# Performance work log

Hardware: AMD Instinct MI355X
Metric: run time of the kernel (lower is better)

Reference implementation:

```python
import jax, jax.numpy as jnp
import numpy as np

HIDDEN = 2048
N_HEADS = 16
N_KV_HEADS = 4
HEAD_DIM = HIDDEN // N_HEADS  # 128
BATCH = 2
SEQ = 2048


def setup_inputs() -> dict:
    key = jax.random.key(0)
    ks = jax.random.split(key, 10)
    s = 0.02
    return {
        "hidden_states": jax.random.normal(ks[0], (BATCH, SEQ, HIDDEN), jnp.float32),
        "attention_mask": jnp.ones((BATCH, SEQ), jnp.int32),
        # weights stored [in, out] so y = x @ W + b (transpose of torch layout)
        "Wq": jax.random.normal(ks[1], (HIDDEN, N_HEADS * HEAD_DIM), jnp.float32) * s,
        "bq": jnp.zeros((N_HEADS * HEAD_DIM,), jnp.float32),
        "Wk": jax.random.normal(ks[2], (HIDDEN, N_KV_HEADS * HEAD_DIM), jnp.float32) * s,
        "bk": jnp.zeros((N_KV_HEADS * HEAD_DIM,), jnp.float32),
        "Wv": jax.random.normal(ks[3], (HIDDEN, N_KV_HEADS * HEAD_DIM), jnp.float32) * s,
        "bv": jnp.zeros((N_KV_HEADS * HEAD_DIM,), jnp.float32),
        "Wo": jax.random.normal(ks[4], (N_HEADS * HEAD_DIM, HIDDEN), jnp.float32) * s,
        "bo": jnp.zeros((HIDDEN,), jnp.float32),
    }


def reference(hidden_states, attention_mask, Wq, bq, Wk, bk, Wv, bv, Wo, bo):
    B, S, _ = hidden_states.shape
    q = hidden_states @ Wq + bq  # [B,S,H*D]
    k = hidden_states @ Wk + bk  # [B,S,Hkv*D]
    v = hidden_states @ Wv + bv

    q = q.reshape(B, S, N_HEADS, HEAD_DIM).transpose(0, 2, 1, 3)      # [B,H,S,D]
    k = k.reshape(B, S, N_KV_HEADS, HEAD_DIM).transpose(0, 2, 1, 3)   # [B,Hkv,S,D]
    v = v.reshape(B, S, N_KV_HEADS, HEAD_DIM).transpose(0, 2, 1, 3)

    # GQA: repeat_interleave along head dim (head h uses kv head h // groups)
    groups = N_HEADS // N_KV_HEADS
    k = jnp.repeat(k, groups, axis=1)  # [B,H,S,D]
    v = jnp.repeat(v, groups, axis=1)

    scale = 1.0 / np.sqrt(HEAD_DIM)
    scores = jnp.einsum('bhqd,bhkd->bhqk', q, k) * scale  # [B,H,S,S]

    causal = jnp.tril(jnp.ones((S, S), bool))              # True = keep
    keep = causal[None, None, :, :] & (attention_mask[:, None, None, :] != 0)
    scores = jnp.where(keep, scores, -jnp.inf)

    attn = jax.nn.softmax(scores.astype(jnp.float32), axis=-1).astype(q.dtype)
    out = jnp.einsum('bhqk,bhkd->bhqd', attn, v)            # [B,H,S,D]
    out = out.transpose(0, 2, 1, 3).reshape(B, S, N_HEADS * HEAD_DIM)
    return out @ Wo + bo
```

## Files before the change

kernel.cpp:

```cpp
#include <hip/hip_runtime.h>
#include <hip/hip_bf16.h>


typedef unsigned short u16;
typedef unsigned long long u64;
typedef __attribute__((ext_vector_type(8))) short short8;
typedef __attribute__((ext_vector_type(4))) float f32x4;
typedef __attribute__((ext_vector_type(4))) unsigned uint4v;

#define BATCH 2
#define SEQ 2048
#define HIDDEN 2048
#define NH 16
#define NKV 4
#define HD 128
#define QKV_N 3072
#define MROWS 4096

__device__ inline u16 f2bf(float f) {
    __hip_bfloat16 h = __float2bfloat16(f);
    return __builtin_bit_cast(u16, h);
}

__device__ inline void async_copy16(const u16* g, u16* lds_base) {
    __builtin_amdgcn_global_load_lds(
        (const __attribute__((address_space(1))) void*)g,
        (__attribute__((address_space(3))) void*)lds_base, 16, 0, 0);
}

#define PREP_CONV   8192
#define PREP_WQ     (PREP_CONV + 4096)
#define PREP_WK     (PREP_WQ + 1024)
#define PREP_WV     (PREP_WK + 1024)
#define PREP_WO     (PREP_WV + 4096)
#define PREP_BIAS   (PREP_WO + 12)
#define PREP_TOTAL  (PREP_BIAS + 1)

__device__ inline void prep_transpose(const float* __restrict__ src, u16* __restrict__ dst,
                                      int N, int sub, float (*tile)[33]) {
    int nx = N >> 5;
    int bx = sub % nx, by = sub / nx;
    int n0 = bx * 32, k0 = by * 32;
    int t = threadIdx.x, tx = t & 31, ty = t >> 5;
#pragma unroll
    for (int i = 0; i < 32; i += 8)
        tile[ty + i][tx] = src[(size_t)(k0 + ty + i) * N + n0 + tx];
    __syncthreads();
#pragma unroll
    for (int i = 0; i < 32; i += 8)
        dst[(size_t)(n0 + ty + i) * HIDDEN + k0 + tx] = f2bf(tile[tx][ty + i]);
}

__global__ __launch_bounds__(256)
void prep(const float* __restrict__ hidden, u16* __restrict__ xb,
          const float* __restrict__ Wq, const float* __restrict__ Wk,
          const float* __restrict__ Wv, const float* __restrict__ Wo,
          u16* __restrict__ wqkvT, u16* __restrict__ woT,
          const float* __restrict__ bq, const float* __restrict__ bk,
          const float* __restrict__ bv, float* __restrict__ bqkv,
          const int* __restrict__ am, u64* __restrict__ mp) {
    __shared__ float tile[32][33];
    int bid = blockIdx.x;
    if (bid < PREP_CONV) {
        int i = (bid * 256 + threadIdx.x) * 4;
        float4 v = *(const float4*)(hidden + i);
        ushort4 o;
        o.x = f2bf(v.x); o.y = f2bf(v.y); o.z = f2bf(v.z); o.w = f2bf(v.w);
        *(ushort4*)(xb + i) = o;
    } else if (bid < PREP_WQ) {
        prep_transpose(Wq, wqkvT, 2048, bid - PREP_CONV, tile);
    } else if (bid < PREP_WK) {
        prep_transpose(Wk, wqkvT + (size_t)2048 * HIDDEN, 512, bid - PREP_WQ, tile);
    } else if (bid < PREP_WV) {
        prep_transpose(Wv, wqkvT + (size_t)2560 * HIDDEN, 512, bid - PREP_WK, tile);
    } else if (bid < PREP_WO) {
        prep_transpose(Wo, woT, 2048, bid - PREP_WV, tile);
    } else if (bid < PREP_BIAS) {
        int i = (bid - PREP_WO) * 256 + threadIdx.x;
        if (i < QKV_N)
            bqkv[i] = (i < 2048) ? bq[i] : ((i < 2560) ? bk[i - 2048] : bv[i - 2560]);
    } else {
        int i = threadIdx.x;
        if (i < BATCH * SEQ / 64) {
            const int* a = am + i * 64;
            u64 m = 0;
#pragma unroll
            for (int j = 0; j < 64; j += 4) {
                int4 v = *(const int4*)(a + j);
                m |= ((u64)(v.x != 0) << j) | ((u64)(v.y != 0) << (j + 1)) |
                     ((u64)(v.z != 0) << (j + 2)) | ((u64)(v.w != 0) << (j + 3));
            }
            mp[i] = m;
        }
    }
}

__global__ void vt_from_qkv(const u16* __restrict__ qkv, u16* __restrict__ vt) {
    __shared__ u16 tile[32][33];
    int b = blockIdx.z >> 2, kvh = blockIdx.z & 3;
    int s0 = blockIdx.x * 32, d0 = blockIdx.y * 32;
    int tx = threadIdx.x, ty = threadIdx.y;
#pragma unroll
    for (int i = 0; i < 32; i += 8)
        tile[ty + i][tx] = qkv[(size_t)(b * SEQ + s0 + ty + i) * QKV_N + 2560 + kvh * HD + d0 + tx];
    __syncthreads();
#pragma unroll
    for (int i = 0; i < 32; i += 8)
        vt[(size_t)((b * NKV + kvh) * HD + d0 + ty + i) * SEQ + s0 + tx] = tile[tx][ty + i];
}

template <bool OUT_BF16>
__global__ __launch_bounds__(256)
void gemm_bf16_128(const u16* __restrict__ A, const u16* __restrict__ BT,
                   const float* __restrict__ bias, void* __restrict__ outp,
                   int M, int N, int K) {
    __shared__ __align__(16) u16 As[128][32];
    __shared__ __align__(16) u16 Bs[128][32];
    int t = threadIdx.x, w = t >> 6, lane = t & 63, quad = lane >> 4, l16 = lane & 15;
    int wm = w & 1, wn = w >> 1;
    int bm0 = blockIdx.y * 128, bn0 = blockIdx.x * 128;

    f32x4 acc[4][4];
#pragma unroll
    for (int i = 0; i < 4; i++)
#pragma unroll
        for (int j = 0; j < 4; j++) acc[i][j] = (f32x4){0.f, 0.f, 0.f, 0.f};

    for (int k0 = 0; k0 < K; k0 += 32) {
        __syncthreads();
#pragma unroll
        for (int j = 0; j < 2; j++) {
            int f = (w * 2 + j) * 64 + lane;
            int row = f >> 2, col = (f & 3) * 8;
            u16* abase = &As[0][0] + (size_t)(w * 2 + j) * 512;
            u16* bbase = &Bs[0][0] + (size_t)(w * 2 + j) * 512;
            async_copy16(A + (size_t)(bm0 + row) * K + k0 + col, abase);
            async_copy16(BT + (size_t)(bn0 + row) * K + k0 + col, bbase);
        }
        __syncthreads();
        short8 af[4], bf[4];
#pragma unroll
        for (int mt = 0; mt < 4; mt++) af[mt] = *(const short8*)(&As[wm * 64 + mt * 16 + l16][quad * 8]);
#pragma unroll
        for (int nt = 0; nt < 4; nt++) bf[nt] = *(const short8*)(&Bs[wn * 64 + nt * 16 + l16][quad * 8]);
#pragma unroll
        for (int mt = 0; mt < 4; mt++)
#pragma unroll
            for (int nt = 0; nt < 4; nt++)
                acc[mt][nt] = __builtin_amdgcn_mfma_f32_16x16x32_bf16(af[mt], bf[nt], acc[mt][nt], 0, 0, 0);
    }
#pragma unroll
    for (int nt = 0; nt < 4; nt++) {
        int col = bn0 + wn * 64 + nt * 16 + l16;
        float bcol = bias[col];
#pragma unroll
        for (int mt = 0; mt < 4; mt++) {
#pragma unroll
            for (int r = 0; r < 4; r++) {
                int row = bm0 + wm * 64 + mt * 16 + quad * 4 + r;
                float v = acc[mt][nt][r] + bcol;
                if constexpr (OUT_BF16)
                    ((u16*)outp)[(size_t)row * N + col] = f2bf(v);
                else
                    ((float*)outp)[(size_t)row * N + col] = v;
            }
        }
    }
}

__global__ __launch_bounds__(512, 4)
void flash_attn(const u16* __restrict__ qkv, const u16* __restrict__ vt,
                const u64* __restrict__ mp, u16* __restrict__ attn) {
    __shared__ __align__(16) u16 Ks[64][136];
    __shared__ __align__(16) u16 Vs[128][72];
    int t = threadIdx.x, w = t >> 6, lane = t & 63, quad = lane >> 4, l16 = lane & 15;
    int bx = blockIdx.x, b = blockIdx.z;
    int qt = b ? ((int)gridDim.x - 1 - bx) : bx;
    int h = blockIdx.y, kvh = h >> 2;
    int q_row0 = qt * 128 + w * 16;

    const u16* qrow = qkv + (size_t)(b * SEQ + q_row0 + l16) * QKV_N + h * HD;
    short8 qf[4];
#pragma unroll
    for (int c = 0; c < 4; c++) qf[c] = *(const short8*)(qrow + c * 32 + quad * 8);

    f32x4 o[8];
#pragma unroll
    for (int dt = 0; dt < 8; dt++) o[dt] = (f32x4){0.f, 0.f, 0.f, 0.f};
    float lpart = 0.f;

    const float scale2 = 0.12751743f;
    const float C2 = 14.4269504f;

    const u16* kgb = qkv + (size_t)(b * SEQ) * QKV_N + 2048 + kvh * HD;
    const u16* vgb = vt + (size_t)((b * NKV + kvh) * HD) * SEQ;
    const u64* mpb = mp + b * (SEQ / 64);

    int kr = t >> 4, kc = (t & 15) * 8;
    int vr = t >> 3, vc = (t & 7) * 8;
    int kb_end = (qt + 1) * 128;

    short8 k0p, k1p, v0p, v1p;
    {
        k0p = *(const short8*)(kgb + (size_t)kr * QKV_N + kc);
        k1p = *(const short8*)(kgb + (size_t)(kr + 32) * QKV_N + kc);
        v0p = *(const short8*)(vgb + (size_t)vr * SEQ + vc);
        v1p = *(const short8*)(vgb + (size_t)(vr + 64) * SEQ + vc);
    }

    for (int kb = 0; kb < kb_end; kb += 64) {
        __syncthreads();
        *(short8*)(&Ks[kr][kc]) = k0p;
        *(short8*)(&Ks[kr + 32][kc]) = k1p;
        *(short8*)(&Vs[vr][vc]) = v0p;
        *(short8*)(&Vs[vr + 64][vc]) = v1p;
        __syncthreads();
        if (kb + 64 < kb_end) {
            const u16* kg = kgb + (size_t)(kb + 64) * QKV_N;
            const u16* vg = vgb + kb + 64;
            k0p = *(const short8*)(kg + (size_t)kr * QKV_N + kc);
            k1p = *(const short8*)(kg + (size_t)(kr + 32) * QKV_N + kc);
            v0p = *(const short8*)(vg + (size_t)vr * SEQ + vc);
            v1p = *(const short8*)(vg + (size_t)(vr + 64) * SEQ + vc);
        }
        if (kb > q_row0 + 15) continue;

        u64 mk = mpb[kb >> 6];

        f32x4 sc[4];
#pragma unroll
        for (int nt = 0; nt < 4; nt++) sc[nt] = (f32x4){0.f, 0.f, 0.f, 0.f};
        __builtin_amdgcn_s_setprio(1);
#pragma unroll
        for (int c = 0; c < 4; c++) {
#pragma unroll
            for (int nt = 0; nt < 4; nt++) {
                short8 kf = *(const short8*)(&Ks[nt * 16 + l16][c * 32 + quad * 8]);
                sc[nt] = __builtin_amdgcn_mfma_f32_16x16x32_bf16(kf, qf[c], sc[nt], 0, 0, 0);
            }
        }
        __builtin_amdgcn_s_setprio(0);

        short8 vf0a[4];
#pragma unroll
        for (int dt = 0; dt < 4; dt++)
            vf0a[dt] = *(const short8*)(&Vs[dt * 16 + l16][quad * 8]);

        int limit = q_row0 + l16 - kb;
        float p[4][4];
#pragma unroll
        for (int nt = 0; nt < 4; nt++) {
            unsigned nib = (unsigned)(mk >> (nt * 16 + quad * 4));
#pragma unroll
            for (int r = 0; r < 4; r++) {
                int bp = nt * 16 + quad * 4 + r;
                bool ok = ((nib >> r) & 1u) && (bp <= limit);
                float v = ok ? sc[nt][r] : -INFINITY;
                p[nt][r] = __builtin_exp2f(__builtin_fmaf(v, scale2, -C2));
            }
        }
        lpart += ((p[0][0] + p[0][1]) + (p[0][2] + p[0][3])) +
                 ((p[1][0] + p[1][1]) + (p[1][2] + p[1][3])) +
                 ((p[2][0] + p[2][1]) + (p[2][2] + p[2][3])) +
                 ((p[3][0] + p[3][1]) + (p[3][2] + p[3][3]));

        unsigned A0, A1, B0, B1, C0, C1, E0, E1;
        asm("v_cvt_pk_bf16_f32 %0, %1, %2" : "=v"(A0) : "v"(p[0][0]), "v"(p[0][1]));
        asm("v_cvt_pk_bf16_f32 %0, %1, %2" : "=v"(A1) : "v"(p[0][2]), "v"(p[0][3]));
        asm("v_cvt_pk_bf16_f32 %0, %1, %2" : "=v"(B0) : "v"(p[1][0]), "v"(p[1][1]));
        asm("v_cvt_pk_bf16_f32 %0, %1, %2" : "=v"(B1) : "v"(p[1][2]), "v"(p[1][3]));
        asm("v_cvt_pk_bf16_f32 %0, %1, %2" : "=v"(C0) : "v"(p[2][0]), "v"(p[2][1]));
        asm("v_cvt_pk_bf16_f32 %0, %1, %2" : "=v"(C1) : "v"(p[2][2]), "v"(p[2][3]));
        asm("v_cvt_pk_bf16_f32 %0, %1, %2" : "=v"(E0) : "v"(p[3][0]), "v"(p[3][1]));
        asm("v_cvt_pk_bf16_f32 %0, %1, %2" : "=v"(E1) : "v"(p[3][2]), "v"(p[3][3]));
        asm("v_permlane32_swap_b32 %0, %1" : "+v"(A0), "+v"(B0));
        asm("v_permlane16_swap_b32 %0, %1" : "+v"(A0), "+v"(B0));
        asm("v_permlane32_swap_b32 %0, %1" : "+v"(A1), "+v"(B1));
        asm("v_permlane16_swap_b32 %0, %1" : "+v"(A1), "+v"(B1));
        asm("v_permlane32_swap_b32 %0, %1" : "+v"(C0), "+v"(E0));
        asm("v_permlane16_swap_b32 %0, %1" : "+v"(C0), "+v"(E0));
        asm("v_permlane32_swap_b32 %0, %1" : "+v"(C1), "+v"(E1));
        asm("v_permlane16_swap_b32 %0, %1" : "+v"(C1), "+v"(E1));
        short8 pf0 = __builtin_bit_cast(short8, (uint4v){A0, A1, B0, B1});
        short8 pf1 = __builtin_bit_cast(short8, (uint4v){C0, C1, E0, E1});

        __builtin_amdgcn_s_setprio(1);
#pragma unroll
        for (int dt = 0; dt < 4; dt++)
            o[dt] = __builtin_amdgcn_mfma_f32_16x16x32_bf16(pf0, vf0a[dt], o[dt], 0, 0, 0);
#pragma unroll
        for (int dt = 4; dt < 8; dt++) {
            short8 vf0 = *(const short8*)(&Vs[dt * 16 + l16][quad * 8]);
            o[dt] = __builtin_amdgcn_mfma_f32_16x16x32_bf16(pf0, vf0, o[dt], 0, 0, 0);
        }
#pragma unroll
        for (int dt = 0; dt < 8; dt++) {
            short8 vf1 = *(const short8*)(&Vs[dt * 16 + l16][32 + quad * 8]);
            o[dt] = __builtin_amdgcn_mfma_f32_16x16x32_bf16(pf1, vf1, o[dt], 0, 0, 0);
        }
        __builtin_amdgcn_s_setprio(0);
    }
    float l = lpart;
    l += __shfl_xor(l, 16, 64);
    l += __shfl_xor(l, 32, 64);
    float invq[4];
#pragma unroll
    for (int r = 0; r < 4; r++) {
        float lr = __shfl(l, quad * 4 + r, 16);
        invq[r] = lr > 0.f ? 1.f / lr : 0.f;
    }
    size_t obase = (size_t)(b * SEQ + q_row0) * HIDDEN + h * HD;
#pragma unroll
    for (int dt = 0; dt < 8; dt++)
#pragma unroll
        for (int r = 0; r < 4; r++)
            attn[obase + (size_t)(quad * 4 + r) * HIDDEN + dt * 16 + l16] =
                f2bf(o[dt][r] * invq[r]);
}

extern "C" void kernel_launch(void* const* d_in, const int* in_sizes, int n_in,
                              void* d_out, int out_size, void* d_ws, size_t ws_size,
                              hipStream_t stream) {
    const float* hidden = (const float*)d_in[0];
    const int* amask   = (const int*)d_in[1];
    const float* Wq = (const float*)d_in[2];
    const float* bq = (const float*)d_in[3];
    const float* Wk = (const float*)d_in[4];
    const float* bk = (const float*)d_in[5];
    const float* Wv = (const float*)d_in[6];
    const float* bv = (const float*)d_in[7];
    const float* Wo = (const float*)d_in[8];
    const float* bo = (const float*)d_in[9];
    float* out = (float*)d_out;

    char* ws = (char*)d_ws;
    u16* xb     = (u16*)ws;  ws += (size_t)MROWS * HIDDEN * 2;
    u16* wqkvT  = (u16*)ws;  ws += (size_t)QKV_N * HIDDEN * 2;
    u16* woT    = (u16*)ws;  ws += (size_t)HIDDEN * HIDDEN * 2;
    float* bqkv = (float*)ws; ws += (size_t)QKV_N * 4;
    u64* mpk    = (u64*)ws;  ws += (size_t)(MROWS / 64) * 8;
    u16* qkv    = (u16*)ws;  ws += (size_t)MROWS * QKV_N * 2;
    u16* vt     = (u16*)ws;  ws += (size_t)BATCH * NKV * HD * SEQ * 2;
    u16* attn   = (u16*)ws;  ws += (size_t)MROWS * HIDDEN * 2;

    prep<<<dim3(PREP_TOTAL), dim3(256), 0, stream>>>(
        hidden, xb, Wq, Wk, Wv, Wo, wqkvT, woT, bq, bk, bv, bqkv, amask, mpk);

    gemm_bf16_128<true><<<dim3(QKV_N / 128, MROWS / 128), dim3(256), 0, stream>>>(
        xb, wqkvT, bqkv, qkv, MROWS, QKV_N, HIDDEN);

    vt_from_qkv<<<dim3(SEQ / 32, HD / 32, BATCH * NKV), dim3(32, 8), 0, stream>>>(qkv, vt);

    flash_attn<<<dim3(SEQ / 128, NH, BATCH), dim3(512), 0, stream>>>(qkv, vt, mpk, attn);

    gemm_bf16_128<false><<<dim3(HIDDEN / 128, MROWS / 128), dim3(256), 0, stream>>>(
        attn, woT, bo, out, MROWS, HIDDEN, HIDDEN);
}
```

Baseline: 318.0 us.

## Rewrite GEMM as 256x256 double-buffered tile with swizzled LDS and prefetch

Replaces the 128x128, 4-wave GEMM, which synchronized twice per K=32 step, with a 256x256, 8-wave kernel. It double-buffers K=64 LDS stages and issues async copies for the next stage while MFMAs run on the current one, split into quarters with partial vmcnt waits. LDS chunks are XOR-swizzled to avoid bank conflicts, and s_setprio boosts MFMA issue. The larger tile gives more reuse per load, but the grids shrink to 192 and 128 blocks, which may underfill the 256 CUs of the MI355X.

```diff
diff --git a/kernel.cpp b/kernel.cpp
--- a/kernel.cpp
+++ b/kernel.cpp
@@ -110,54 +110,123 @@
 }
 
 template <bool OUT_BF16>
-__global__ __launch_bounds__(256)
-void gemm_bf16_128(const u16* __restrict__ A, const u16* __restrict__ BT,
+__global__ __launch_bounds__(512, 2)
+void gemm_bf16_256(const u16* __restrict__ A, const u16* __restrict__ BT,
                    const float* __restrict__ bias, void* __restrict__ outp,
                    int M, int N, int K) {
-    __shared__ __align__(16) u16 As[128][32];
-    __shared__ __align__(16) u16 Bs[128][32];
-    int t = threadIdx.x, w = t >> 6, lane = t & 63, quad = lane >> 4, l16 = lane & 15;
-    int wm = w & 1, wn = w >> 1;
-    int bm0 = blockIdx.y * 128, bn0 = blockIdx.x * 128;
-
-    f32x4 acc[4][4];
-#pragma unroll
-    for (int i = 0; i < 4; i++)
+    __shared__ __align__(16) u16 smem[2][2][256][64];
+    const int t = threadIdx.x, w = t >> 6, lane = t & 63;
+    const int quad = lane >> 4, l16 = lane & 15;
+    const int wm = w >> 2, wn = w & 3;
+    const int bm0 = blockIdx.y * 256, bn0 = blockIdx.x * 256;
+    const int lrow = lane >> 3;
+    const int lchk = (lane & 7) ^ lrow;
+    const int NT = K >> 6;
+
+    f32x4 acc[8][4];
+#pragma unroll
+    for (int i = 0; i < 8; i++)
 #pragma unroll
         for (int j = 0; j < 4; j++) acc[i][j] = (f32x4){0.f, 0.f, 0.f, 0.f};
 
-    for (int k0 = 0; k0 < K; k0 += 32) {
-        __syncthreads();
-#pragma unroll
-        for (int j = 0; j < 2; j++) {
-            int f = (w * 2 + j) * 64 + lane;
-            int row = f >> 2, col = (f & 3) * 8;
-            u16* abase = &As[0][0] + (size_t)(w * 2 + j) * 512;
-            u16* bbase = &Bs[0][0] + (size_t)(w * 2 + j) * 512;
-            async_copy16(A + (size_t)(bm0 + row) * K + k0 + col, abase);
-            async_copy16(BT + (size_t)(bn0 + row) * K + k0 + col, bbase);
-        }
-        __syncthreads();
-        short8 af[4], bf[4];
-#pragma unroll
-        for (int mt = 0; mt < 4; mt++) af[mt] = *(const short8*)(&As[wm * 64 + mt * 16 + l16][quad * 8]);
-#pragma unroll
-        for (int nt = 0; nt < 4; nt++) bf[nt] = *(const short8*)(&Bs[wn * 64 + nt * 16 + l16][quad * 8]);
-#pragma unroll
-        for (int mt = 0; mt < 4; mt++)
-#pragma unroll
-            for (int nt = 0; nt < 4; nt++)
-                acc[mt][nt] = __builtin_amdgcn_mfma_f32_16x16x32_bf16(af[mt], bf[nt], acc[mt][nt], 0, 0, 0);
-    }
-#pragma unroll
-    for (int nt = 0; nt < 4; nt++) {
-        int col = bn0 + wn * 64 + nt * 16 + l16;
+    const u16* gA = A + (size_t)bm0 * K;
+    const u16* gB = BT + (size_t)bn0 * K;
+
+    auto stage = [&](int buf, int op, int h, int k0) {
+        const u16* gb = op ? gB : gA;
+#pragma unroll
+        for (int l = 0; l < 2; ++l) {
+            int rb = h * 128 + w * 16 + l * 8;
+            async_copy16(gb + (size_t)(rb + lrow) * K + k0 + lchk * 8,
+                         &smem[buf][op][rb][0]);
+        }
+    };
+    auto readA = [&](short8 (&aq)[4][2], int buf, int mh) {
+#pragma unroll
+        for (int mt = 0; mt < 4; ++mt) {
+            int row = mh * 128 + mt * 32 + wm * 16 + l16;
+            int swz = row & 7;
+#pragma unroll
+            for (int kk = 0; kk < 2; ++kk) {
+                int chunk = ((kk << 2) | quad) ^ swz;
+                aq[mt][kk] = *(const short8*)(&smem[buf][0][row][chunk << 3]);
+            }
+        }
+    };
+    auto readB = [&](short8 (&bq)[2][2], int buf, int nh) {
+#pragma unroll
+        for (int nt = 0; nt < 2; ++nt) {
+            int row = nh * 128 + nt * 64 + wn * 16 + l16;
+            int swz = row & 7;
+#pragma unroll
+            for (int kk = 0; kk < 2; ++kk) {
+                int chunk = ((kk << 2) | quad) ^ swz;
+                bq[nt][kk] = *(const short8*)(&smem[buf][1][row][chunk << 3]);
+            }
+        }
+    };
+    auto mmaQ = [&](short8 (&aq)[4][2], short8 (&bq)[2][2], int mh, int nh) {
+        __builtin_amdgcn_s_setprio(1);
+#pragma unroll
+        for (int mt = 0; mt < 4; ++mt)
+#pragma unroll
+            for (int nt = 0; nt < 2; ++nt)
+#pragma unroll
+                for (int kk = 0; kk < 2; ++kk)
+                    acc[mh * 4 + mt][nh * 2 + nt] = __builtin_amdgcn_mfma_f32_16x16x32_bf16(
+                        aq[mt][kk], bq[nt][kk], acc[mh * 4 + mt][nh * 2 + nt], 0, 0, 0);
+        __builtin_amdgcn_s_setprio(0);
+    };
+
+    stage(0, 0, 0, 0); stage(0, 1, 0, 0); stage(0, 1, 1, 0); stage(0, 0, 1, 0);
+    asm volatile("s_waitcnt vmcnt(4)" ::: "memory");
+    __builtin_amdgcn_s_barrier();
+
+    short8 aq[4][2], b0[2][2], b1[2][2];
+    for (int tt = 0; tt < NT - 1; ++tt) {
+        const int cur = tt & 1, nxt = cur ^ 1, k1 = (tt + 1) << 6;
+        readA(aq, cur, 0); readB(b0, cur, 0);
+        stage(nxt, 0, 0, k1);
+        mmaQ(aq, b0, 0, 0);
+        asm volatile("s_waitcnt vmcnt(4)" ::: "memory");
+        __builtin_amdgcn_s_barrier();
+        readB(b1, cur, 1);
+        stage(nxt, 1, 0, k1);
+        mmaQ(aq, b1, 0, 1);
+        asm volatile("s_waitcnt vmcnt(4)" ::: "memory");
+        __builtin_amdgcn_s_barrier();
+        readA(aq, cur, 1);
+        stage(nxt, 1, 1, k1);
+        mmaQ(aq, b1, 1, 1);
+        asm volatile("s_waitcnt vmcnt(6)" ::: "memory");
+        __builtin_amdgcn_s_barrier();
+        stage(nxt, 0, 1, k1);
+        mmaQ(aq, b0, 1, 0);
+        asm volatile("s_waitcnt vmcnt(4)" ::: "memory");
+        __builtin_amdgcn_s_barrier();
+    }
+    asm volatile("s_waitcnt vmcnt(0)" ::: "memory");
+    __builtin_amdgcn_s_barrier();
+    {
+        const int cur = (NT - 1) & 1;
+        readA(aq, cur, 0); readB(b0, cur, 0);
+        mmaQ(aq, b0, 0, 0);
+        readB(b1, cur, 1);
+        mmaQ(aq, b1, 0, 1);
+        readA(aq, cur, 1);
+        mmaQ(aq, b1, 1, 1);
+        mmaQ(aq, b0, 1, 0);
+    }
+
+#pragma unroll
+    for (int nt = 0; nt < 4; ++nt) {
+        int col = bn0 + nt * 64 + wn * 16 + l16;
         float bcol = bias[col];
 #pragma unroll
-        for (int mt = 0; mt < 4; mt++) {
-#pragma unroll
-            for (int r = 0; r < 4; r++) {
-                int row = bm0 + wm * 64 + mt * 16 + quad * 4 + r;
+        for (int mt = 0; mt < 8; ++mt) {
+#pragma unroll
+            for (int r = 0; r < 4; ++r) {
+                int row = bm0 + mt * 32 + wm * 16 + quad * 4 + r;
                 float v = acc[mt][nt][r] + bcol;
                 if constexpr (OUT_BF16)
                     ((u16*)outp)[(size_t)row * N + col] = f2bf(v);
@@ -346,13 +415,13 @@
     prep<<<dim3(PREP_TOTAL), dim3(256), 0, stream>>>(
         hidden, xb, Wq, Wk, Wv, Wo, wqkvT, woT, bq, bk, bv, bqkv, amask, mpk);
 
-    gemm_bf16_128<true><<<dim3(QKV_N / 128, MROWS / 128), dim3(256), 0, stream>>>(
+    gemm_bf16_256<true><<<dim3(QKV_N / 256, MROWS / 256), dim3(512), 0, stream>>>(
         xb, wqkvT, bqkv, qkv, MROWS, QKV_N, HIDDEN);
 
     vt_from_qkv<<<dim3(SEQ / 32, HD / 32, BATCH * NKV), dim3(32, 8), 0, stream>>>(qkv, vt);
 
     flash_attn<<<dim3(SEQ / 128, NH, BATCH), dim3(512), 0, stream>>>(qkv, vt, mpk, attn);
 
-    gemm_bf16_128<false><<<dim3(HIDDEN / 128, MROWS / 128), dim3(256), 0, stream>>>(
+    gemm_bf16_256<false><<<dim3(HIDDEN / 256, MROWS / 256), dim3(512), 0, stream>>>(
         attn, woT, bo, out, MROWS, HIDDEN, HIDDEN);
 }
```

After: 298.5 us. 6.1% less time.
